# Kernel optimization log

Hardware: AMD Instinct MI355X
Metric: run time of the kernel (lower is better)

The kernel has to match this reference:

```python
import jax, jax.numpy as jnp
import numpy as np

B, H, W = 8, 640, 640
NUM_INST = 16  # upper bound on instance ids; segment reduce handles absent ids


def _bce(p, t):
    # torch BCELoss clamps log terms at -100
    lp = jnp.clip(jnp.log(p), -100.0)
    l1p = jnp.clip(jnp.log1p(-p), -100.0)
    return -(t * lp + (1.0 - t) * l1p)


def setup_inputs() -> dict:
    key = jax.random.key(0)
    k1, k2, k3, k4 = jax.random.split(key, 4)
    preds = jax.random.uniform(k1, (B, 2, H, W), dtype=jnp.float32,
                               minval=1e-4, maxval=1.0 - 1e-4)
    conf = jax.random.bernoulli(k2, 0.3, (B, H, W)).astype(jnp.float32)
    overlap = jax.random.bernoulli(k3, 0.1, (B, H, W)).astype(jnp.float32)
    inst = jax.random.randint(k4, (B, H, W), 0, NUM_INST, dtype=jnp.int32)
    inds = jnp.arange(B, dtype=jnp.int64) if jax.config.jax_enable_x64 else jnp.arange(B, dtype=jnp.int32)
    return {"preds": preds, "conf": conf, "inst": inst,
            "overlap": overlap, "inds": inds}


def reference(preds, conf, inst, overlap, inds):
    p1 = preds[:, 0]
    p2 = preds[:, 1]
    and_preds = p1 * p2
    and_loss_map = _bce(and_preds, overlap)            # [B,H,W]
    or_loss = _bce(jnp.maximum(p1, p2), conf).mean()
    and_overlap = and_preds * overlap
    op1 = jnp.maximum(p1, and_overlap)
    op2 = jnpp = jnp.maximum(p2, and_overlap)

    b, h, w = p1.shape
    # per-(sample, instance-id) segment reduce replacing the python loops.
    # MSELoss(bop*mask, mask)/sum(mask) == segment-mean of (op-1)^2 over the mask.
    seg = (jnp.arange(b, dtype=jnp.int32)[:, None, None] * NUM_INST + inst).reshape(-1)
    e1 = ((op1 - 1.0) ** 2).reshape(-1)
    e2 = ((op2 - 1.0) ** 2).reshape(-1)
    nseg = b * NUM_INST
    cnt = jax.ops.segment_sum(jnp.ones_like(e1), seg, num_segments=nseg).reshape(b, NUM_INST)
    s1 = jax.ops.segment_sum(e1, seg, num_segments=nseg).reshape(b, NUM_INST)
    s2 = jax.ops.segment_sum(e2, seg, num_segments=nseg).reshape(b, NUM_INST)
    present = cnt > 0
    safe_cnt = jnp.where(present, cnt, 1.0)
    d1 = s1 / safe_cnt
    d2 = s2 / safe_cnt
    # min(d1,d2) - max(d1,d2) + 1 == 1 - |d1 - d2|, only for present keys
    per_key = jnp.where(present, 1.0 - jnp.abs(d1 - d2), 0.0)
    nkeys = present.sum(axis=1).astype(p1.dtype)       # torch.unique count per sample
    inst_loss = (per_key.sum(axis=1) / nkeys).mean()

    pos = (conf == 1).astype(p1.dtype)
    neg = (conf == 0).astype(p1.dtype)
    and_loss = (and_loss_map * pos).sum() / pos.sum() + (and_loss_map * neg).sum() / neg.sum()

    return 0.5 * and_loss + 0.25 * or_loss + 0.25 * inst_loss
```

## Files before the change

### kernel.cpp

```cpp
#include <hip/hip_runtime.h>
#include <hip/hip_bf16.h>

#define BB 8
#define HH 640
#define WW 640
#define HWN (HH * WW)
#define NUM_INST 16
#define NBLK 128
#define NBLK_TOT (NBLK * BB)
#define THREADS 256
#define NV 36


__device__ __forceinline__ void process_pixel(
    float p1, float p2, float c, float t, int k,
    float* s12, unsigned* cnt_s,
    float& lgPos, float& lgAll, float& lgOr, float& accCnt)
{
    float andp = p1 * p2;
    bool tpos = (t != 0.0f);
    bool cpos = (c != 0.0f);
    float argA = tpos ? andp : (1.0f - andp);
    float lg = __logf(argA);
    lgAll += lg;
    lgPos = fmaf(c, lg, lgPos);
    accCnt += c;
    float mx = fmaxf(p1, p2);
    float argO = cpos ? mx : (1.0f - mx);
    lgOr += __logf(argO);
    float ao = t * andp;
    float d1 = fmaxf(p1, ao) - 1.0f;
    float d2 = fmaxf(p2, ao) - 1.0f;
    float e12 = (d1 - d2) * (d1 + d2);
    #pragma unroll
    for (int j = 0; j < NUM_INST; ++j) {
        bool m = (k == j);
        s12[j] += m ? e12 : 0.0f;
        cnt_s[j] += (unsigned)__popcll(__ballot(m));
    }
}

__global__ __launch_bounds__(THREADS) void overlap_main_kernel(
    const float* __restrict__ preds, const float* __restrict__ conf,
    const int* __restrict__ inst, const float* __restrict__ overlap,
    float* __restrict__ ws)
{
    const int b   = blockIdx.y;
    const int tid = threadIdx.x;

    const float4* p1v = (const float4*)(preds + (size_t)b * 2 * HWN);
    const float4* p2v = (const float4*)(preds + (size_t)b * 2 * HWN + HWN);
    const float4* cv  = (const float4*)(conf    + (size_t)b * HWN);
    const float4* tv  = (const float4*)(overlap + (size_t)b * HWN);
    const int4*   kv  = (const int4*)(inst      + (size_t)b * HWN);

    float s12[NUM_INST];
    unsigned cnt_s[NUM_INST];
    #pragma unroll
    for (int j = 0; j < NUM_INST; ++j) { s12[j] = 0.0f; cnt_s[j] = 0u; }
    float lgPos = 0.0f, lgAll = 0.0f, lgOr = 0.0f, accCnt = 0.0f;

    const int nvec   = HWN / 4;
    const int stride = NBLK * THREADS;
    for (int i = blockIdx.x * THREADS + tid; i < nvec; i += stride) {
        float4 A = p1v[i];
        float4 B = p2v[i];
        float4 C = cv[i];
        float4 T = tv[i];
        int4   K = kv[i];
        process_pixel(A.x, B.x, C.x, T.x, K.x, s12, cnt_s, lgPos, lgAll, lgOr, accCnt);
        process_pixel(A.y, B.y, C.y, T.y, K.y, s12, cnt_s, lgPos, lgAll, lgOr, accCnt);
        process_pixel(A.z, B.z, C.z, T.z, K.z, s12, cnt_s, lgPos, lgAll, lgOr, accCnt);
        process_pixel(A.w, B.w, C.w, T.w, K.w, s12, cnt_s, lgPos, lgAll, lgOr, accCnt);
    }

    float fv[20];
    #pragma unroll
    for (int j = 0; j < NUM_INST; ++j) fv[j] = s12[j];
    fv[16] = lgPos; fv[17] = lgAll; fv[18] = lgOr; fv[19] = accCnt;
    #pragma unroll
    for (int s = 32; s > 0; s >>= 1) {
        #pragma unroll
        for (int v = 0; v < 20; ++v) fv[v] += __shfl_xor(fv[v], s, 64);
    }

    __shared__ float wsum[4][NV];
    const int wave = tid >> 6;
    const int lane = tid & 63;
    if (lane == 0) {
        #pragma unroll
        for (int j = 0; j < NUM_INST; ++j) {
            wsum[wave][j]      = fv[j];
            wsum[wave][16 + j] = (float)cnt_s[j];
        }
        wsum[wave][32] = -fv[16];
        wsum[wave][33] = -fv[17];
        wsum[wave][34] = -fv[18];
        wsum[wave][35] = fv[19];
    }
    __syncthreads();
    if (tid < NV) {
        float s = wsum[0][tid] + wsum[1][tid] + wsum[2][tid] + wsum[3][tid];
        int g = blockIdx.y * NBLK + blockIdx.x;
        ws[tid * NBLK_TOT + g] = s;
    }
}

__global__ __launch_bounds__(320) void overlap_finalize_kernel(
    const float* __restrict__ ws, float* __restrict__ out)
{
    __shared__ float seg[BB][NV];
    __shared__ float perkey[BB][NUM_INST];
    __shared__ float pres[BB][NUM_INST];
    __shared__ float binst[BB];
    const int t = threadIdx.x;

    if (t < BB * NV) {
        int b = t / NV, v = t - (t / NV) * NV;
        const float4* p = (const float4*)(ws + v * NBLK_TOT + b * NBLK);
        float4 s4 = {0.0f, 0.0f, 0.0f, 0.0f};
        #pragma unroll 8
        for (int i = 0; i < NBLK / 4; ++i) {
            float4 q = p[i];
            s4.x += q.x; s4.y += q.y; s4.z += q.z; s4.w += q.w;
        }
        seg[b][v] = (s4.x + s4.y) + (s4.z + s4.w);
    }
    __syncthreads();

    if (t < BB * NUM_INST) {
        int b = t >> 4, k = t & 15;
        float c = seg[b][16 + k];
        bool present = c > 0.0f;
        float sc = present ? c : 1.0f;
        perkey[b][k] = present ? (1.0f - fabsf(seg[b][k]) / sc) : 0.0f;
        pres[b][k]   = present ? 1.0f : 0.0f;
    }
    __syncthreads();

    if (t < BB) {
        float s = 0.0f, nk = 0.0f;
        for (int k = 0; k < NUM_INST; ++k) { s += perkey[t][k]; nk += pres[t][k]; }
        binst[t] = s / nk;
    }
    __syncthreads();

    if (t == 0) {
        float instLoss = 0.0f, posS = 0.0f, allS = 0.0f, orS = 0.0f, posC = 0.0f;
        for (int b = 0; b < BB; ++b) {
            instLoss += binst[b];
            posS += seg[b][32];
            allS += seg[b][33];
            orS  += seg[b][34];
            posC += seg[b][35];
        }
        instLoss *= (1.0f / (float)BB);
        const float N = (float)BB * (float)HWN;
        float negS = allS - posS;
        float andLoss = posS / posC + negS / (N - posC);
        float orLoss  = orS / N;
        out[0] = 0.5f * andLoss + 0.25f * orLoss + 0.25f * instLoss;
    }
}

extern "C" void kernel_launch(void* const* d_in, const int* in_sizes, int n_in,
                              void* d_out, int out_size, void* d_ws, size_t ws_size,
                              hipStream_t stream) {
    const float* preds   = (const float*)d_in[0];
    const float* conf    = (const float*)d_in[1];
    const int*   inst    = (const int*)d_in[2];
    const float* overlap = (const float*)d_in[3];
    float* ws  = (float*)d_ws;
    float* out = (float*)d_out;

    dim3 grid(NBLK, BB);
    overlap_main_kernel<<<grid, THREADS, 0, stream>>>(preds, conf, inst, overlap, ws);
    overlap_finalize_kernel<<<1, 320, 0, stream>>>(ws, out);
}
```

Measured before the change: 110.1 us.

## Replace per-instance ballot loop with per-thread shared-memory histogram bins

Each pixel's instance contribution now goes into a per-thread column of a shared-memory histogram [16][256] through atomicAdd. This replaces the previous 16-way unrolled compare, select and ballot/popcount per pixel. Logs switch to log2 with a single ln2 rescale at the end, and blocks now cover contiguous ranges instead of a grid stride. The cost is 32 KB of LDS per block, which may limit occupancy, plus LDS atomics. Counts are now float sums, and each thread reads back its 32 columns before the shuffle reduction, which now reduces 36 values instead of 20.

New measurement: 137.9 us. +25.2%, slower.

```diff
diff --git a/kernel.cpp b/kernel.cpp
--- a/kernel.cpp
+++ b/kernel.cpp
@@ -1,5 +1,4 @@
 #include <hip/hip_runtime.h>
-#include <hip/hip_bf16.h>
 
 #define BB 8
 #define HH 640
@@ -10,34 +9,30 @@
 #define NBLK_TOT (NBLK * BB)
 #define THREADS 256
 #define NV 36
+#define NVEC (HWN / 4)
+#define VPB (NVEC / NBLK)
 
 
 __device__ __forceinline__ void process_pixel(
-    float p1, float p2, float c, float t, int k,
-    float* s12, unsigned* cnt_s,
+    float p1, float p2, float c, float t, int k, int tid,
+    float (&s_e)[NUM_INST][THREADS], float (&s_c)[NUM_INST][THREADS],
     float& lgPos, float& lgAll, float& lgOr, float& accCnt)
 {
     float andp = p1 * p2;
-    bool tpos = (t != 0.0f);
-    bool cpos = (c != 0.0f);
-    float argA = tpos ? andp : (1.0f - andp);
-    float lg = __logf(argA);
+    float argA = (t != 0.0f) ? andp : (1.0f - andp);
+    float lg = __log2f(argA);
     lgAll += lg;
     lgPos = fmaf(c, lg, lgPos);
     accCnt += c;
     float mx = fmaxf(p1, p2);
-    float argO = cpos ? mx : (1.0f - mx);
-    lgOr += __logf(argO);
+    float argO = (c != 0.0f) ? mx : (1.0f - mx);
+    lgOr += __log2f(argO);
     float ao = t * andp;
     float d1 = fmaxf(p1, ao) - 1.0f;
     float d2 = fmaxf(p2, ao) - 1.0f;
     float e12 = (d1 - d2) * (d1 + d2);
-    #pragma unroll
-    for (int j = 0; j < NUM_INST; ++j) {
-        bool m = (k == j);
-        s12[j] += m ? e12 : 0.0f;
-        cnt_s[j] += (unsigned)__popcll(__ballot(m));
-    }
+    atomicAdd(&s_e[k][tid], e12);
+    atomicAdd(&s_c[k][tid], 1.0f);
 }
 
 __global__ __launch_bounds__(THREADS) void overlap_main_kernel(
@@ -45,62 +40,59 @@
     const int* __restrict__ inst, const float* __restrict__ overlap,
     float* __restrict__ ws)
 {
+    __shared__ float s_e[NUM_INST][THREADS];
+    __shared__ float s_c[NUM_INST][THREADS];
+    __shared__ float wsum[4][NV];
+
     const int b   = blockIdx.y;
     const int tid = threadIdx.x;
 
+    #pragma unroll
+    for (int j = 0; j < NUM_INST; ++j) { s_e[j][tid] = 0.0f; s_c[j][tid] = 0.0f; }
+
     const float4* p1v = (const float4*)(preds + (size_t)b * 2 * HWN);
-    const float4* p2v = (const float4*)(preds + (size_t)b * 2 * HWN + HWN);
+    const float4* p2v = p1v + NVEC;
     const float4* cv  = (const float4*)(conf    + (size_t)b * HWN);
     const float4* tv  = (const float4*)(overlap + (size_t)b * HWN);
     const int4*   kv  = (const int4*)(inst      + (size_t)b * HWN);
 
-    float s12[NUM_INST];
-    unsigned cnt_s[NUM_INST];
-    #pragma unroll
-    for (int j = 0; j < NUM_INST; ++j) { s12[j] = 0.0f; cnt_s[j] = 0u; }
     float lgPos = 0.0f, lgAll = 0.0f, lgOr = 0.0f, accCnt = 0.0f;
 
-    const int nvec   = HWN / 4;
-    const int stride = NBLK * THREADS;
-    for (int i = blockIdx.x * THREADS + tid; i < nvec; i += stride) {
+    const int lim = (blockIdx.x + 1) * VPB;
+    for (int i = blockIdx.x * VPB + tid; i < lim; i += THREADS) {
         float4 A = p1v[i];
-        float4 B = p2v[i];
+        float4 Bv = p2v[i];
         float4 C = cv[i];
         float4 T = tv[i];
         int4   K = kv[i];
-        process_pixel(A.x, B.x, C.x, T.x, K.x, s12, cnt_s, lgPos, lgAll, lgOr, accCnt);
-        process_pixel(A.y, B.y, C.y, T.y, K.y, s12, cnt_s, lgPos, lgAll, lgOr, accCnt);
-        process_pixel(A.z, B.z, C.z, T.z, K.z, s12, cnt_s, lgPos, lgAll, lgOr, accCnt);
-        process_pixel(A.w, B.w, C.w, T.w, K.w, s12, cnt_s, lgPos, lgAll, lgOr, accCnt);
+        process_pixel(A.x, Bv.x, C.x, T.x, K.x, tid, s_e, s_c, lgPos, lgAll, lgOr, accCnt);
+        process_pixel(A.y, Bv.y, C.y, T.y, K.y, tid, s_e, s_c, lgPos, lgAll, lgOr, accCnt);
+        process_pixel(A.z, Bv.z, C.z, T.z, K.z, tid, s_e, s_c, lgPos, lgAll, lgOr, accCnt);
+        process_pixel(A.w, Bv.w, C.w, T.w, K.w, tid, s_e, s_c, lgPos, lgAll, lgOr, accCnt);
     }
 
-    float fv[20];
+    float fv[NV];
     #pragma unroll
-    for (int j = 0; j < NUM_INST; ++j) fv[j] = s12[j];
-    fv[16] = lgPos; fv[17] = lgAll; fv[18] = lgOr; fv[19] = accCnt;
+    for (int j = 0; j < NUM_INST; ++j) { fv[j] = s_e[j][tid]; fv[16 + j] = s_c[j][tid]; }
+    fv[32] = lgPos; fv[33] = lgAll; fv[34] = lgOr; fv[35] = accCnt;
+
     #pragma unroll
     for (int s = 32; s > 0; s >>= 1) {
         #pragma unroll
-        for (int v = 0; v < 20; ++v) fv[v] += __shfl_xor(fv[v], s, 64);
+        for (int v = 0; v < NV; ++v) fv[v] += __shfl_xor(fv[v], s, 64);
     }
 
-    __shared__ float wsum[4][NV];
     const int wave = tid >> 6;
     const int lane = tid & 63;
     if (lane == 0) {
         #pragma unroll
-        for (int j = 0; j < NUM_INST; ++j) {
-            wsum[wave][j]      = fv[j];
-            wsum[wave][16 + j] = (float)cnt_s[j];
-        }
-        wsum[wave][32] = -fv[16];
-        wsum[wave][33] = -fv[17];
-        wsum[wave][34] = -fv[18];
-        wsum[wave][35] = fv[19];
+        for (int v = 0; v < NV; ++v) wsum[wave][v] = fv[v];
     }
     __syncthreads();
     if (tid < NV) {
         float s = wsum[0][tid] + wsum[1][tid] + wsum[2][tid] + wsum[3][tid];
+        if (tid >= 32 && tid < 35)
+            s = -0.69314718055994530942f * s;
         int g = blockIdx.y * NBLK + blockIdx.x;
         ws[tid * NBLK_TOT + g] = s;
     }
```
